# Performance work log

Hardware: AMD Instinct MI355X
Metric: run time of the kernel (lower is better)

The kernel has to match this reference:

```python
import jax, jax.numpy as jnp
import numpy as np

EPS = 1e-16


def setup_inputs() -> dict:
    key = jax.random.key(0)
    k1, k2 = jax.random.split(key)
    N, D = 512, 4096
    a = jax.random.normal(k1, (N, D), dtype=jnp.float32)
    p = jax.random.normal(k2, (N, D), dtype=jnp.float32)
    return {"a": a, "p": p}


def reference(a, p):
    N = a.shape[0]
    # Pairwise squared distances between anchors a and positives p:
    # ||a_i||^2 - 2 a_i . p_j + ||p_j||^2   (diag(a a^T) == row norms)
    dot = jnp.matmul(a, p.T)                       # [N, N]
    sq_a = jnp.sum(a * a, axis=-1)                 # [N]
    sq_p = jnp.sum(p * p, axis=-1)                 # [N]
    d2 = sq_a[:, None] - 2.0 * dot + sq_p[None, :]
    d2 = jnp.maximum(d2, 0.0)                      # distances[distances < 0] = 0
    zero_mask = (d2 == 0.0).astype(d2.dtype)
    dist = (1.0 - zero_mask) * jnp.sqrt(d2 + zero_mask * EPS)  # [N, N]

    # Triplet tensor: loss[a, p, n] = dist[a, p] - dist[a, n]
    triplet = dist[:, :, None] - dist[:, None, :]  # [N, N, N]

    # Validity mask: labels = arange(N) -> valid iff p == anchor and n != anchor
    labels = jnp.arange(N)
    label_eq = labels[:, None] == labels[None, :]  # [N, N]
    mask = label_eq[:, :, None] & (~label_eq[:, None, :])  # [N, N, N]

    triplet = mask.astype(triplet.dtype) * triplet
    triplet = jax.nn.relu(triplet)

    num_positive = jnp.sum(triplet > EPS).astype(triplet.dtype)
    loss = jnp.sum(triplet) / (num_positive + EPS)
    return loss
```

## Files before the change

kernel.cpp:

```cpp
#include <hip/hip_runtime.h>
#include <math.h>

#define PN 512
#define PD 4096

#define KSZ 8
#define KCHUNK (PD / KSZ)
#define BK 64
#define NSTAGE (KCHUNK / BK)

#define WS_AH_BYTES 8192
#define WS_PH_BYTES (8192 + 4194304)
#define WS_PART_FLOAT 2099200
#define WS_NEED_BF16 ((size_t)(8192 + 2 * 4194304 + (size_t)KSZ * PN * PN * 4))

typedef __attribute__((ext_vector_type(8))) short short8;
typedef __attribute__((ext_vector_type(4))) float floatx4;

static __device__ __forceinline__ unsigned short f2bf(float x) {
    unsigned int u = __float_as_uint(x);
    u += 0x7fffu + ((u >> 16) & 1u);
    return (unsigned short)(u >> 16);
}

static __device__ __forceinline__ void load16_lds(const void* gp, void* lp) {
    __builtin_amdgcn_global_load_lds(
        (const __attribute__((address_space(1))) unsigned int*)gp,
        (__attribute__((address_space(3))) unsigned int*)lp,
        16, 0, 0);
}

struct ushort4s { unsigned short x, y, z, w; };

__global__ __launch_bounds__(256) void taw_prep_kernel(
        const float* __restrict__ a, const float* __restrict__ p,
        float* __restrict__ ws) {
    const int i = blockIdx.x;
    const int t = threadIdx.x;
    if (i == 0 && t == 0) {
        ws[1536] = 0.0f;
        ((unsigned int*)ws)[1537] = 0u;
    }
    const float4* a4 = (const float4*)(a + (size_t)i * PD);
    const float4* p4 = (const float4*)(p + (size_t)i * PD);
    unsigned short* ah = (unsigned short*)((char*)ws + WS_AH_BYTES) + (size_t)i * PD;
    unsigned short* ph = (unsigned short*)((char*)ws + WS_PH_BYTES) + (size_t)i * PD;
    float sa = 0.f, sp = 0.f, dp = 0.f;
#pragma unroll
    for (int c = 0; c < 4; ++c) {
        const int e = c * 256 + t;
        float4 av = a4[e];
        float4 pv = p4[e];
        sa += av.x * av.x + av.y * av.y + av.z * av.z + av.w * av.w;
        sp += pv.x * pv.x + pv.y * pv.y + pv.z * pv.z + pv.w * pv.w;
        dp += av.x * pv.x + av.y * pv.y + av.z * pv.z + av.w * pv.w;
        ushort4s ab = {f2bf(av.x), f2bf(av.y), f2bf(av.z), f2bf(av.w)};
        ushort4s pb = {f2bf(pv.x), f2bf(pv.y), f2bf(pv.z), f2bf(pv.w)};
        *(ushort4s*)(ah + (size_t)e * 4) = ab;
        *(ushort4s*)(ph + (size_t)e * 4) = pb;
    }
#pragma unroll
    for (int off = 32; off > 0; off >>= 1) {
        sa += __shfl_down(sa, off, 64);
        sp += __shfl_down(sp, off, 64);
        dp += __shfl_down(dp, off, 64);
    }
    __shared__ float red[3][4];
    const int wave = t >> 6;
    if ((t & 63) == 0) { red[0][wave] = sa; red[1][wave] = sp; red[2][wave] = dp; }
    __syncthreads();
    if (t == 0) {
        sa = red[0][0] + red[0][1] + red[0][2] + red[0][3];
        sp = red[1][0] + red[1][1] + red[1][2] + red[1][3];
        dp = red[2][0] + red[2][1] + red[2][2] + red[2][3];
        float d2 = sa - 2.f * dp + sp;
        d2 = fmaxf(d2, 0.f);
        ws[i] = sa;
        ws[512 + i] = sp;
        ws[1024 + i] = (d2 == 0.f) ? 0.f : sqrtf(d2);
    }
}

__global__ __launch_bounds__(256) void taw_mfma_kernel(float* __restrict__ ws) {
    __shared__ short lds[2][8][64][8];
    const unsigned short* ah = (const unsigned short*)((const char*)ws + WS_AH_BYTES);
    const unsigned short* ph = (const unsigned short*)((const char*)ws + WS_PH_BYTES);
    const int t = threadIdx.x;
    const int lane = t & 63;
    const int w = t >> 6;
    const int wm = w >> 1, wn = w & 1;
    const int i0 = blockIdx.y * 64;
    const int j0 = blockIdx.x * 64;
    const int kz = blockIdx.z * KCHUNK;

    floatx4 acc[2][2] = {{{0.f, 0.f, 0.f, 0.f}, {0.f, 0.f, 0.f, 0.f}},
                         {{0.f, 0.f, 0.f, 0.f}, {0.f, 0.f, 0.f, 0.f}}};

    for (int st = 0; st < NSTAGE; ++st) {
        const int kb = kz + st * BK;
        __syncthreads();
#pragma unroll
        for (int q = 0; q < 2; ++q) {
            const int g = 2 * w + q;
            const int row = ((g & 3) << 4) + (lane & 15);
            const int kk = kb + ((((g >> 2) << 2) + (lane >> 4)) << 3);
            load16_lds(ah + (size_t)(i0 + row) * PD + kk, &lds[0][g][0][0]);
            load16_lds(ph + (size_t)(j0 + row) * PD + kk, &lds[1][g][0][0]);
        }
        __syncthreads();
#pragma unroll
        for (int s2 = 0; s2 < 2; ++s2) {
            short8 af0 = *(const short8*)&lds[0][s2 * 4 + wm * 2 + 0][lane][0];
            short8 af1 = *(const short8*)&lds[0][s2 * 4 + wm * 2 + 1][lane][0];
            short8 bf0 = *(const short8*)&lds[1][s2 * 4 + wn * 2 + 0][lane][0];
            short8 bf1 = *(const short8*)&lds[1][s2 * 4 + wn * 2 + 1][lane][0];
            acc[0][0] = __builtin_amdgcn_mfma_f32_16x16x32_bf16(af0, bf0, acc[0][0], 0, 0, 0);
            acc[0][1] = __builtin_amdgcn_mfma_f32_16x16x32_bf16(af0, bf1, acc[0][1], 0, 0, 0);
            acc[1][0] = __builtin_amdgcn_mfma_f32_16x16x32_bf16(af1, bf0, acc[1][0], 0, 0, 0);
            acc[1][1] = __builtin_amdgcn_mfma_f32_16x16x32_bf16(af1, bf1, acc[1][1], 0, 0, 0);
        }
    }

    float* part = ws + WS_PART_FLOAT + (size_t)blockIdx.z * (PN * PN);
    const int jj = j0 + wn * 32 + (lane & 15);
    const int ib = i0 + wm * 32 + ((lane >> 4) << 2);
#pragma unroll
    for (int rm = 0; rm < 2; ++rm)
#pragma unroll
        for (int rn = 0; rn < 2; ++rn)
#pragma unroll
            for (int r = 0; r < 4; ++r)
                part[(size_t)(ib + rm * 16 + r) * PN + jj + rn * 16] = acc[rm][rn][r];
}

__global__ __launch_bounds__(256) void taw_reduce_kernel(float* __restrict__ ws) {
    const int g = blockIdx.x * 256 + threadIdx.x;
    const float4* part4 = (const float4*)(ws + WS_PART_FLOAT);
    float4 dot = part4[g];
#pragma unroll
    for (int ks = 1; ks < KSZ; ++ks) {
        const float4 v = part4[((size_t)ks << 16) + g];
        dot.x += v.x; dot.y += v.y; dot.z += v.z; dot.w += v.w;
    }
    const int flat = g << 2;
    const int i = flat >> 9;
    const int j = flat & 511;
    const float sa = ws[i];
    const float dd = ws[1024 + i];
    const float4 sp4 = *(const float4*)(ws + 512 + j);
    const float dotr[4] = {dot.x, dot.y, dot.z, dot.w};
    const float spr[4] = {sp4.x, sp4.y, sp4.z, sp4.w};
    float lsum = 0.f;
    unsigned int lcnt = 0;
#pragma unroll
    for (int c = 0; c < 4; ++c) {
        const int jj = j + c;
        float d2 = sa - 2.f * dotr[c] + spr[c];
        d2 = fmaxf(d2, 0.f);
        const float dist = (d2 == 0.f) ? 0.f : sqrtf(d2);
        const float v = (i != jj) ? fmaxf(dd - dist, 0.f) : 0.f;
        lsum += v;
        lcnt += (v > 1e-16f) ? 1u : 0u;
    }
#pragma unroll
    for (int off = 32; off > 0; off >>= 1) {
        lsum += __shfl_down(lsum, off, 64);
        lcnt += __shfl_down(lcnt, off, 64);
    }
    __shared__ float rsum[4];
    __shared__ unsigned int rcnt[4];
    const int t = threadIdx.x;
    if ((t & 63) == 0) { rsum[t >> 6] = lsum; rcnt[t >> 6] = lcnt; }
    __syncthreads();
    if (t == 0) {
        atomicAdd(ws + 1536, rsum[0] + rsum[1] + rsum[2] + rsum[3]);
        atomicAdd(((unsigned int*)ws) + 1537, rcnt[0] + rcnt[1] + rcnt[2] + rcnt[3]);
    }
}

__global__ void taw_finalize_kernel(const float* __restrict__ ws,
                                    float* __restrict__ out) {
    const double s = (double)ws[1536];
    const double c = (double)(((const unsigned int*)ws)[1537]);
    out[0] = (float)(s / (c + 1e-16));
}

__global__ __launch_bounds__(256) void taw_gemm_loss_kernel(
        const float* __restrict__ A, const float* __restrict__ P,
        float* __restrict__ ws) {
    __shared__ float as[32][34];
    __shared__ float bs[32][34];
    const int tx = threadIdx.x;
    const int ty = threadIdx.y;
    const int t = ty * 16 + tx;
    const int i0 = blockIdx.y * 32;
    const int j0 = blockIdx.x * 32;
    const int sr = t >> 3;
    const int sk = (t & 7) * 4;
    const float* aptr = A + (size_t)(i0 + sr) * PD + sk;
    const float* pptr = P + (size_t)(j0 + sr) * PD + sk;
    float c00 = 0.f, c01 = 0.f, c10 = 0.f, c11 = 0.f;
    for (int k0 = 0; k0 < PD; k0 += 32) {
        float4 av = *(const float4*)(aptr + k0);
        float4 pv = *(const float4*)(pptr + k0);
        __syncthreads();
        as[sk + 0][sr] = av.x; as[sk + 1][sr] = av.y;
        as[sk + 2][sr] = av.z; as[sk + 3][sr] = av.w;
        bs[sk + 0][sr] = pv.x; bs[sk + 1][sr] = pv.y;
        bs[sk + 2][sr] = pv.z; bs[sk + 3][sr] = pv.w;
        __syncthreads();
#pragma unroll
        for (int kk = 0; kk < 32; ++kk) {
            const float2 a2 = *(const float2*)&as[kk][2 * ty];
            const float2 b2 = *(const float2*)&bs[kk][2 * tx];
            c00 = fmaf(a2.x, b2.x, c00);
            c01 = fmaf(a2.x, b2.y, c01);
            c10 = fmaf(a2.y, b2.x, c10);
            c11 = fmaf(a2.y, b2.y, c11);
        }
    }
    const float* sq_a = ws;
    const float* sq_p = ws + 512;
    const float* ddg  = ws + 1024;
    const int i = i0 + 2 * ty;
    const int j = j0 + 2 * tx;
    float cvals[2][2] = {{c00, c01}, {c10, c11}};
    float lsum = 0.f;
    unsigned int lcnt = 0;
#pragma unroll
    for (int dr = 0; dr < 2; ++dr)
#pragma unroll
        for (int dc = 0; dc < 2; ++dc) {
            const int ii = i + dr, jj = j + dc;
            float d2 = sq_a[ii] - 2.f * cvals[dr][dc] + sq_p[jj];
            d2 = fmaxf(d2, 0.f);
            const float dist = (d2 == 0.f) ? 0.f : sqrtf(d2);
            const float v = (ii != jj) ? fmaxf(ddg[ii] - dist, 0.f) : 0.f;
            lsum += v;
            lcnt += (v > 1e-16f) ? 1u : 0u;
        }
#pragma unroll
    for (int off = 32; off > 0; off >>= 1) {
        lsum += __shfl_down(lsum, off, 64);
        lcnt += __shfl_down(lcnt, off, 64);
    }
    __shared__ float rsum[4];
    __shared__ unsigned int rcnt[4];
    if ((t & 63) == 0) { rsum[t >> 6] = lsum; rcnt[t >> 6] = lcnt; }
    __syncthreads();
    if (t == 0) {
        atomicAdd(ws + 1536, rsum[0] + rsum[1] + rsum[2] + rsum[3]);
        atomicAdd(((unsigned int*)ws) + 1537, rcnt[0] + rcnt[1] + rcnt[2] + rcnt[3]);
    }
}

extern "C" void kernel_launch(void* const* d_in, const int* in_sizes, int n_in,
                              void* d_out, int out_size, void* d_ws, size_t ws_size,
                              hipStream_t stream) {
    (void)in_sizes; (void)n_in; (void)out_size;
    const float* a = (const float*)d_in[0];
    const float* p = (const float*)d_in[1];
    float* out = (float*)d_out;
    float* ws = (float*)d_ws;

    taw_prep_kernel<<<PN, 256, 0, stream>>>(a, p, ws);
    if (ws_size >= WS_NEED_BF16) {
        taw_mfma_kernel<<<dim3(8, 8, KSZ), 256, 0, stream>>>(ws);
        taw_reduce_kernel<<<256, 256, 0, stream>>>(ws);
    } else {
        taw_gemm_loss_kernel<<<dim3(16, 16), dim3(16, 16), 0, stream>>>(a, p, ws);
    }
    taw_finalize_kernel<<<1, 1, 0, stream>>>(ws, out);
}
```

Measured before the change: 89.56 us.

## Fuse split-K reduction and finalize into MFMA kernel via last-block atomics

```diff
diff --git a/kernel.cpp b/kernel.cpp
--- a/kernel.cpp
+++ b/kernel.cpp
@@ -9,10 +9,17 @@
 #define BK 64
 #define NSTAGE (KCHUNK / BK)
 
+#define F_SA 0
+#define F_SP 512
+#define F_DD 1024
+#define F_SUM 1536
+#define F_CNT 1537
+#define F_DONE 1538
+#define F_TILECNT 1600
 #define WS_AH_BYTES 8192
 #define WS_PH_BYTES (8192 + 4194304)
 #define WS_PART_FLOAT 2099200
-#define WS_NEED_BF16 ((size_t)(8192 + 2 * 4194304 + (size_t)KSZ * PN * PN * 4))
+#define WS_NEED ((size_t)WS_PART_FLOAT * 4 + (size_t)64 * KSZ * 4096 * 4)
 
 typedef __attribute__((ext_vector_type(8))) short short8;
 typedef __attribute__((ext_vector_type(4))) float floatx4;
@@ -37,10 +44,7 @@
         float* __restrict__ ws) {
     const int i = blockIdx.x;
     const int t = threadIdx.x;
-    if (i == 0 && t == 0) {
-        ws[1536] = 0.0f;
-        ((unsigned int*)ws)[1537] = 0u;
-    }
+    if (i == 0 && t < 128) ((unsigned int*)ws)[1536 + t] = 0u;
     const float4* a4 = (const float4*)(a + (size_t)i * PD);
     const float4* p4 = (const float4*)(p + (size_t)i * PD);
     unsigned short* ah = (unsigned short*)((char*)ws + WS_AH_BYTES) + (size_t)i * PD;
@@ -75,13 +79,14 @@
         dp = red[2][0] + red[2][1] + red[2][2] + red[2][3];
         float d2 = sa - 2.f * dp + sp;
         d2 = fmaxf(d2, 0.f);
-        ws[i] = sa;
-        ws[512 + i] = sp;
-        ws[1024 + i] = (d2 == 0.f) ? 0.f : sqrtf(d2);
-    }
-}
-
-__global__ __launch_bounds__(256) void taw_mfma_kernel(float* __restrict__ ws) {
+        ws[F_SA + i] = sa;
+        ws[F_SP + i] = sp;
+        ws[F_DD + i] = (d2 == 0.f) ? 0.f : sqrtf(d2);
+    }
+}
+
+__global__ __launch_bounds__(256) void taw_fused_kernel(float* __restrict__ ws,
+                                                        float* __restrict__ out) {
     __shared__ short lds[2][8][64][8];
     const unsigned short* ah = (const unsigned short*)((const char*)ws + WS_AH_BYTES);
     const unsigned short* ph = (const unsigned short*)((const char*)ws + WS_PH_BYTES);
@@ -91,13 +96,15 @@
     const int wm = w >> 1, wn = w & 1;
     const int i0 = blockIdx.y * 64;
     const int j0 = blockIdx.x * 64;
-    const int kz = blockIdx.z * KCHUNK;
+    const int tile = blockIdx.y * 8 + blockIdx.x;
+    const int kzb = blockIdx.z * KCHUNK;
+    unsigned int* wsu = (unsigned int*)ws;
 
     floatx4 acc[2][2] = {{{0.f, 0.f, 0.f, 0.f}, {0.f, 0.f, 0.f, 0.f}},
                          {{0.f, 0.f, 0.f, 0.f}, {0.f, 0.f, 0.f, 0.f}}};
 
     for (int st = 0; st < NSTAGE; ++st) {
-        const int kb = kz + st * BK;
+        const int kb = kzb + st * BK;
         __syncthreads();
 #pragma unroll
         for (int q = 0; q < 2; ++q) {
@@ -121,46 +128,56 @@
         }
     }
 
-    float* part = ws + WS_PART_FLOAT + (size_t)blockIdx.z * (PN * PN);
-    const int jj = j0 + wn * 32 + (lane & 15);
-    const int ib = i0 + wm * 32 + ((lane >> 4) << 2);
+    float* part = ws + WS_PART_FLOAT + ((size_t)tile * KSZ + blockIdx.z) * 4096;
+    const int jj = wn * 32 + (lane & 15);
+    const int ib = wm * 32 + ((lane >> 4) << 2);
 #pragma unroll
     for (int rm = 0; rm < 2; ++rm)
 #pragma unroll
         for (int rn = 0; rn < 2; ++rn)
 #pragma unroll
             for (int r = 0; r < 4; ++r)
-                part[(size_t)(ib + rm * 16 + r) * PN + jj + rn * 16] = acc[rm][rn][r];
-}
-
-__global__ __launch_bounds__(256) void taw_reduce_kernel(float* __restrict__ ws) {
-    const int g = blockIdx.x * 256 + threadIdx.x;
-    const float4* part4 = (const float4*)(ws + WS_PART_FLOAT);
-    float4 dot = part4[g];
-#pragma unroll
-    for (int ks = 1; ks < KSZ; ++ks) {
-        const float4 v = part4[((size_t)ks << 16) + g];
-        dot.x += v.x; dot.y += v.y; dot.z += v.z; dot.w += v.w;
-    }
-    const int flat = g << 2;
-    const int i = flat >> 9;
-    const int j = flat & 511;
-    const float sa = ws[i];
-    const float dd = ws[1024 + i];
-    const float4 sp4 = *(const float4*)(ws + 512 + j);
-    const float dotr[4] = {dot.x, dot.y, dot.z, dot.w};
-    const float spr[4] = {sp4.x, sp4.y, sp4.z, sp4.w};
+                part[(ib + rm * 16 + r) * 64 + jj + rn * 16] = acc[rm][rn][r];
+
+    __syncthreads();
+    __shared__ unsigned int lastflag;
+    if (t == 0) {
+        __threadfence();
+        lastflag = (atomicAdd(&wsu[F_TILECNT + tile], 1u) == KSZ - 1) ? 1u : 0u;
+    }
+    __syncthreads();
+    if (!lastflag) return;
+
+    const float* pbase = ws + WS_PART_FLOAT + (size_t)tile * KSZ * 4096;
+    const int row = t >> 2;
+    const int c0 = (t & 3) * 16;
+    const int gi = i0 + row;
+    const float sa = ws[F_SA + gi];
+    const float dd = ws[F_DD + gi];
     float lsum = 0.f;
     unsigned int lcnt = 0;
 #pragma unroll
-    for (int c = 0; c < 4; ++c) {
-        const int jj = j + c;
-        float d2 = sa - 2.f * dotr[c] + spr[c];
-        d2 = fmaxf(d2, 0.f);
-        const float dist = (d2 == 0.f) ? 0.f : sqrtf(d2);
-        const float v = (i != jj) ? fmaxf(dd - dist, 0.f) : 0.f;
-        lsum += v;
-        lcnt += (v > 1e-16f) ? 1u : 0u;
+    for (int v = 0; v < 4; ++v) {
+        const int e = row * 64 + c0 + v * 4;
+        float4 d = *(const float4*)(pbase + e);
+#pragma unroll
+        for (int k = 1; k < KSZ; ++k) {
+            const float4 q = *(const float4*)(pbase + k * 4096 + e);
+            d.x += q.x; d.y += q.y; d.z += q.z; d.w += q.w;
+        }
+        const int gj = j0 + c0 + v * 4;
+        const float4 sp4 = *(const float4*)(ws + F_SP + gj);
+        const float dr[4] = {d.x, d.y, d.z, d.w};
+        const float sr[4] = {sp4.x, sp4.y, sp4.z, sp4.w};
+#pragma unroll
+        for (int c = 0; c < 4; ++c) {
+            float d2 = sa - 2.f * dr[c] + sr[c];
+            d2 = fmaxf(d2, 0.f);
+            const float dist = (d2 == 0.f) ? 0.f : sqrtf(d2);
+            const float vv = (gi != gj + c) ? fmaxf(dd - dist, 0.f) : 0.f;
+            lsum += vv;
+            lcnt += (vv > 1e-16f) ? 1u : 0u;
+        }
     }
 #pragma unroll
     for (int off = 32; off > 0; off >>= 1) {
@@ -169,20 +186,19 @@
     }
     __shared__ float rsum[4];
     __shared__ unsigned int rcnt[4];
-    const int t = threadIdx.x;
-    if ((t & 63) == 0) { rsum[t >> 6] = lsum; rcnt[t >> 6] = lcnt; }
-    __syncthreads();
-    if (t == 0) {
-        atomicAdd(ws + 1536, rsum[0] + rsum[1] + rsum[2] + rsum[3]);
-        atomicAdd(((unsigned int*)ws) + 1537, rcnt[0] + rcnt[1] + rcnt[2] + rcnt[3]);
-    }
-}
-
-__global__ void taw_finalize_kernel(const float* __restrict__ ws,
-                                    float* __restrict__ out) {
-    const double s = (double)ws[1536];
-    const double c = (double)(((const unsigned int*)ws)[1537]);
-    out[0] = (float)(s / (c + 1e-16));
+    if (lane == 0) { rsum[w] = lsum; rcnt[w] = lcnt; }
+    __syncthreads();
+    if (t == 0) {
+        atomicAdd(ws + F_SUM, rsum[0] + rsum[1] + rsum[2] + rsum[3]);
+        atomicAdd(&wsu[F_CNT], rcnt[0] + rcnt[1] + rcnt[2] + rcnt[3]);
+        __threadfence();
+        if (atomicAdd(&wsu[F_DONE], 1u) == 63u) {
+            __threadfence();
+            const float s = atomicAdd(ws + F_SUM, 0.0f);
+            const unsigned int c = atomicAdd(&wsu[F_CNT], 0u);
+            out[0] = (float)((double)s / ((double)c + 1e-16));
+        }
+    }
 }
 
 __global__ __launch_bounds__(256) void taw_gemm_loss_kernel(
@@ -219,9 +235,6 @@
             c11 = fmaf(a2.y, b2.y, c11);
         }
     }
-    const float* sq_a = ws;
-    const float* sq_p = ws + 512;
-    const float* ddg  = ws + 1024;
     const int i = i0 + 2 * ty;
     const int j = j0 + 2 * tx;
     float cvals[2][2] = {{c00, c01}, {c10, c11}};
@@ -232,10 +245,10 @@
 #pragma unroll
         for (int dc = 0; dc < 2; ++dc) {
             const int ii = i + dr, jj = j + dc;
-            float d2 = sq_a[ii] - 2.f * cvals[dr][dc] + sq_p[jj];
+            float d2 = ws[F_SA + ii] - 2.f * cvals[dr][dc] + ws[F_SP + jj];
             d2 = fmaxf(d2, 0.f);
             const float dist = (d2 == 0.f) ? 0.f : sqrtf(d2);
-            const float v = (ii != jj) ? fmaxf(ddg[ii] - dist, 0.f) : 0.f;
+            const float v = (ii != jj) ? fmaxf(ws[F_DD + ii] - dist, 0.f) : 0.f;
             lsum += v;
             lcnt += (v > 1e-16f) ? 1u : 0u;
         }
@@ -249,9 +262,16 @@
     if ((t & 63) == 0) { rsum[t >> 6] = lsum; rcnt[t >> 6] = lcnt; }
     __syncthreads();
     if (t == 0) {
-        atomicAdd(ws + 1536, rsum[0] + rsum[1] + rsum[2] + rsum[3]);
-        atomicAdd(((unsigned int*)ws) + 1537, rcnt[0] + rcnt[1] + rcnt[2] + rcnt[3]);
-    }
+        atomicAdd(ws + F_SUM, rsum[0] + rsum[1] + rsum[2] + rsum[3]);
+        atomicAdd(((unsigned int*)ws) + F_CNT, rcnt[0] + rcnt[1] + rcnt[2] + rcnt[3]);
+    }
+}
+
+__global__ void taw_finalize_kernel(const float* __restrict__ ws,
+                                    float* __restrict__ out) {
+    const double s = (double)ws[F_SUM];
+    const double c = (double)(((const unsigned int*)ws)[F_CNT]);
+    out[0] = (float)(s / (c + 1e-16));
 }
 
 extern "C" void kernel_launch(void* const* d_in, const int* in_sizes, int n_in,
@@ -264,11 +284,10 @@
     float* ws = (float*)d_ws;
 
     taw_prep_kernel<<<PN, 256, 0, stream>>>(a, p, ws);
-    if (ws_size >= WS_NEED_BF16) {
-        taw_mfma_kernel<<<dim3(8, 8, KSZ), 256, 0, stream>>>(ws);
-        taw_reduce_kernel<<<256, 256, 0, stream>>>(ws);
+    if (ws_size >= WS_NEED) {
+        taw_fused_kernel<<<dim3(8, 8, KSZ), 256, 0, stream>>>(ws, out);
     } else {
         taw_gemm_loss_kernel<<<dim3(16, 16), dim3(16, 16), 0, stream>>>(a, p, ws);
-    }
-    taw_finalize_kernel<<<1, 1, 0, stream>>>(ws, out);
-}
+        taw_finalize_kernel<<<1, 1, 0, stream>>>(ws, out);
+    }
+}
```

After: 97.84 us. 1.09x slower.
